# Kernel optimization log

Hardware: AMD Instinct MI355X
Metric: run time of the kernel (lower is better)

Reference implementation:

```python
import jax, jax.numpy as jnp
import numpy as np

N = 8192
D = 256  # hidden_size = in_features = out_features
NEG_SLOPE = 0.01  # nn.LeakyReLU() default
MASK_VAL = -1e12


def setup_inputs() -> dict:
    key = jax.random.key(0)
    k1, k2, k3, k4 = jax.random.split(key, 4)
    x = jax.random.normal(k1, (N, D), dtype=jnp.float32)
    adj = jax.random.randint(k2, (N, N), 0, 2, dtype=jnp.int32)
    # kaiming_uniform_ style params (scaled random uniform)
    W = jax.random.normal(k3, (D, D), dtype=jnp.float32) * (1.0 / np.sqrt(D))
    a = jax.random.normal(k4, (2 * D, 1), dtype=jnp.float32) * (1.0 / np.sqrt(2 * D))
    return {"x": x, "adj": adj, "W": W, "a": a}


def reference(x, adj, W, a):
    # GraphAttentionLayer.forward (eval mode: dropout is identity)
    h = x @ W  # [N, D]
    # a_input[i,j] = concat(h_i, h_j); a_input @ a decomposes as:
    #   e[i,j] = h_i . a[:D] + h_j . a[D:]
    # identical math without materializing the [N, N, 2D] tensor.
    e_src = h @ a[:D, 0]  # [N]
    e_dst = h @ a[D:, 0]  # [N]
    e = e_src[:, None] + e_dst[None, :]  # [N, N]
    e = jnp.where(e > 0, e, NEG_SLOPE * e)  # LeakyReLU
    att_logits = jnp.where(adj > 0, e, MASK_VAL)
    attention = jax.nn.softmax(att_logits, axis=1)
    h_prime = attention @ h  # [N, D]
    return jax.nn.elu(h_prime)  # concat=True branch
```

## Files before the change

### kernel.cpp

```cpp
#include <hip/hip_runtime.h>

#define NN 8192
#define DD 256
#define NSTEP (NN / 32)

typedef __attribute__((ext_vector_type(8))) short short8;
typedef __attribute__((ext_vector_type(4))) float f32x4;

__device__ __forceinline__ short f2bf(float x) {
    union { float f; unsigned u; } v; v.f = x;
    unsigned r = (v.u + 0x7FFFu + ((v.u >> 16) & 1u)) >> 16;
    return (short)r;
}
__device__ __forceinline__ float bf2f(short b) {
    union { float f; unsigned u; } v; v.u = ((unsigned)(unsigned short)b) << 16;
    return v.f;
}

__device__ __forceinline__ void barrier_keep_vmem() {
    asm volatile("s_waitcnt lgkmcnt(0)" ::: "memory");
    __builtin_amdgcn_s_barrier();
    asm volatile("" ::: "memory");
}

__global__ __launch_bounds__(256) void gat_pack(
    const int* __restrict__ adj, unsigned* __restrict__ bits)
{
    const int t   = threadIdx.x;
    const int row = blockIdx.x;
    const int* ar = adj + (size_t)row * NN;
    unsigned* br  = bits + (size_t)row * (NN / 32);
    #pragma unroll
    for (int i = 0; i < 8; ++i) {
        int j0 = i * 1024 + t * 4;
        int4 v = *(const int4*)(ar + j0);
        unsigned nib = (v.x > 0 ? 1u : 0u) | (v.y > 0 ? 2u : 0u)
                     | (v.z > 0 ? 4u : 0u) | (v.w > 0 ? 8u : 0u);
        unsigned word = nib << ((t & 7) * 4);
        word |= __shfl_xor((int)word, 1);
        word |= __shfl_xor((int)word, 2);
        word |= __shfl_xor((int)word, 4);
        if ((t & 7) == 0) br[i * 32 + (t >> 3)] = word;
    }
}

__global__ __launch_bounds__(256) void gat_prep(
    const float* __restrict__ x, const float* __restrict__ W,
    const float* __restrict__ a,
    short* __restrict__ hT, float* __restrict__ e_src, float* __restrict__ e_dst)
{
    __shared__ float x_s[32][260];
    __shared__ float W_s[2][16][256];
    const int t  = threadIdx.x;
    const int ib = blockIdx.x * 32;

    #pragma unroll
    for (int rep = 0; rep < 8; ++rep) {
        int fi = rep * 256 + t;
        int r  = fi >> 6;
        int c4 = (fi & 63) * 4;
        float4 v = *(const float4*)(x + (size_t)(ib + r) * DD + c4);
        *(float4*)&x_s[r][c4] = v;
    }
    float4 wp[4];
    #pragma unroll
    for (int q = 0; q < 4; ++q) {
        int fi = q * 256 + t;
        wp[q] = *(const float4*)(W + (size_t)(fi >> 6) * DD + (fi & 63) * 4);
    }
    barrier_keep_vmem();

    const int il = t >> 3;
    const int dg = (t & 7) * 4;
    f32x4 acc[8];
    #pragma unroll
    for (int m = 0; m < 8; ++m) acc[m] = (f32x4){0.f, 0.f, 0.f, 0.f};

    for (int kc = 0; kc < 16; ++kc) {
        const int b = kc & 1;
        #pragma unroll
        for (int q = 0; q < 4; ++q) {
            int fi = q * 256 + t;
            *(float4*)&W_s[b][fi >> 6][(fi & 63) * 4] = wp[q];
        }
        if (kc < 15) {
            #pragma unroll
            for (int q = 0; q < 4; ++q) {
                int fi = q * 256 + t;
                wp[q] = *(const float4*)(W + (size_t)((kc + 1) * 16 + (fi >> 6)) * DD + (fi & 63) * 4);
            }
        }
        barrier_keep_vmem();
        #pragma unroll
        for (int kl = 0; kl < 16; ++kl) {
            float xv = x_s[il][kc * 16 + kl];
            #pragma unroll
            for (int m = 0; m < 8; ++m) {
                float4 wv = *(const float4*)&W_s[b][kl][m * 32 + dg];
                acc[m].x += xv * wv.x; acc[m].y += xv * wv.y;
                acc[m].z += xv * wv.z; acc[m].w += xv * wv.w;
            }
        }
    }

    const int ig = ib + il;
    float p1 = 0.f, p2 = 0.f;
    #pragma unroll
    for (int m = 0; m < 8; ++m) {
        #pragma unroll
        for (int j = 0; j < 4; ++j) {
            int col = m * 32 + dg + j;
            float hv = acc[m][j];
            p1 += hv * a[col];
            p2 += hv * a[DD + col];
            hT[(size_t)col * NN + ig] = f2bf(hv);
        }
    }
    p1 += __shfl_xor(p1, 1); p1 += __shfl_xor(p1, 2); p1 += __shfl_xor(p1, 4);
    p2 += __shfl_xor(p2, 1); p2 += __shfl_xor(p2, 2); p2 += __shfl_xor(p2, 4);
    if ((t & 7) == 0) { e_src[ig] = p1; e_dst[ig] = p2; }
}

__global__ __launch_bounds__(512) void gat_main(
    const unsigned* __restrict__ bits, const short* __restrict__ hT,
    const float* __restrict__ e_src, const float* __restrict__ e_dst,
    float* __restrict__ out)
{
    __shared__ __align__(16) short w_s[2][32][40];
    __shared__ float denom_s[32];

    const int t    = threadIdx.x;
    const int lane = t & 63;
    const int wid  = t >> 6;
    const int ibl  = blockIdx.x * 32;

    const int irow = t >> 4;
    const int jc2  = (t & 15) * 2;
    const float es = e_src[ibl + irow];
    const unsigned* bits_row = bits + (size_t)(ibl + irow) * (NN / 32);

    const int cb   = wid * 32;
    const int arow = lane & 15;
    const int kg8  = (lane >> 4) * 8;
    const short* hB = hT + (size_t)(cb + arow) * NN + kg8;

    float dsum = 0.f;
    f32x4 acc00 = {0.f,0.f,0.f,0.f}, acc01 = acc00, acc10 = acc00, acc11 = acc00;

    unsigned bwA = bits_row[0];
    float2   edA = *(const float2*)(e_dst + jc2);
    int4     b0A = *(const int4*)(hB);
    int4     b1A = *(const int4*)(hB + 16 * NN);
    unsigned bwB = bits_row[1];
    float2   edB = *(const float2*)(e_dst + 32 + jc2);
    int4     b0B = *(const int4*)(hB + 32);
    int4     b1B = *(const int4*)(hB + 16 * NN + 32);

#define MAIN_STEP(BW, ED, B0, B1, n)                                           \
    {                                                                          \
        const int c = (n) & 1;                                                 \
        int4 g0 = B0, g1 = B1;                       \
        float s0 = es + ED.x, s1 = es + ED.y;                                  \
        float l0 = s0 > 0.f ? s0 : 0.01f * s0;                                 \
        float l1 = s1 > 0.f ? s1 : 0.01f * s1;                                 \
        float w0 = ((BW >> jc2) & 1u)       ? __expf(l0) : 0.f;                \
        float w1 = ((BW >> (jc2 + 1)) & 1u) ? __expf(l1) : 0.f;                \
        short b0 = f2bf(w0), b1 = f2bf(w1);                                    \
        dsum += bf2f(b0) + bf2f(b1);    \
        *(unsigned*)&w_s[c][irow][jc2] =                                       \
            (unsigned)(unsigned short)b0 | ((unsigned)(unsigned short)b1 << 16);\
        int jn = (((n) + 2) & (NSTEP - 1)) * 32;         \
        BW = bits_row[jn >> 5];                                                \
        ED = *(const float2*)(e_dst + jn + jc2);                               \
        B0 = *(const int4*)(hB + jn);                                          \
        B1 = *(const int4*)(hB + 16 * NN + jn);                                \
        barrier_keep_vmem();          \
        short8 a0 = *(const short8*)&w_s[c][arow][kg8];                        \
        short8 a1 = *(const short8*)&w_s[c][16 + arow][kg8];                   \
        acc00 = __builtin_amdgcn_mfma_f32_16x16x32_bf16(a0, *(short8*)&g0, acc00, 0, 0, 0);\
        acc01 = __builtin_amdgcn_mfma_f32_16x16x32_bf16(a0, *(short8*)&g1, acc01, 0, 0, 0);\
        acc10 = __builtin_amdgcn_mfma_f32_16x16x32_bf16(a1, *(short8*)&g0, acc10, 0, 0, 0);\
        acc11 = __builtin_amdgcn_mfma_f32_16x16x32_bf16(a1, *(short8*)&g1, acc11, 0, 0, 0);\
    }

    for (int n = 0; n < NSTEP; n += 2) {
        MAIN_STEP(bwA, edA, b0A, b1A, n)
        MAIN_STEP(bwB, edB, b0B, b1B, n + 1)
    }
#undef MAIN_STEP

    dsum += __shfl_xor(dsum, 1);
    dsum += __shfl_xor(dsum, 2);
    dsum += __shfl_xor(dsum, 4);
    dsum += __shfl_xor(dsum, 8);
    if ((t & 15) == 0) denom_s[irow] = dsum;
    __syncthreads();

    const int r4 = (lane >> 4) * 4;
    #pragma unroll
    for (int r = 0; r < 4; ++r) {
        float inv0 = 1.f / denom_s[r4 + r];
        float inv1 = 1.f / denom_s[16 + r4 + r];
        size_t o0 = (size_t)(ibl + r4 + r) * DD + cb + arow;
        size_t o1 = (size_t)(ibl + 16 + r4 + r) * DD + cb + arow;
        float v00 = acc00[r] * inv0; v00 = v00 > 0.f ? v00 : expm1f(v00);
        float v01 = acc01[r] * inv0; v01 = v01 > 0.f ? v01 : expm1f(v01);
        float v10 = acc10[r] * inv1; v10 = v10 > 0.f ? v10 : expm1f(v10);
        float v11 = acc11[r] * inv1; v11 = v11 > 0.f ? v11 : expm1f(v11);
        out[o0]      = v00;
        out[o0 + 16] = v01;
        out[o1]      = v10;
        out[o1 + 16] = v11;
    }
}

extern "C" void kernel_launch(void* const* d_in, const int* in_sizes, int n_in,
                              void* d_out, int out_size, void* d_ws, size_t ws_size,
                              hipStream_t stream) {
    const float* x   = (const float*)d_in[0];
    const int*   adj = (const int*)d_in[1];
    const float* W   = (const float*)d_in[2];
    const float* a   = (const float*)d_in[3];
    float* out = (float*)d_out;

    char* w0 = (char*)d_ws;
    short* hT      = (short*)w0;
    float* esrc    = (float*)(w0 + (size_t)DD * NN * 2);
    float* edst    = esrc + NN;
    unsigned* bits = (unsigned*)(edst + NN);

    gat_pack<<<dim3(NN), dim3(256), 0, stream>>>(adj, bits);
    gat_prep<<<dim3(NN / 32), dim3(256), 0, stream>>>(x, W, a, hT, esrc, edst);
    gat_main<<<dim3(NN / 32), dim3(512), 0, stream>>>(bits, hT, esrc, edst, out);
}
```

Baseline: 221.3 us.

## Split neighbor dimension across waves and reduce partial sums through LDS

Each wave now covers a disjoint eighth of the neighbor columns for all 256 output features, instead of a 32-column output slice across all neighbors. Every wave builds its attention-weight fragments directly in registers, so the per-step LDS write and block barrier go away. Partial accumulators and denominators are then summed across the eight waves through a large LDS exchange buffer before normalization and ELU. The cost is 32 accumulator tiles per lane, which strains registers under the new launch bound of two blocks per CU and may spill, plus a large LDS footprint that can limit occupancy.

Result: faster. 216.4 us (-2.2%).

```diff
diff --git a/kernel.cpp b/kernel.cpp
--- a/kernel.cpp
+++ b/kernel.cpp
@@ -2,7 +2,6 @@
 
 #define NN 8192
 #define DD 256
-#define NSTEP (NN / 32)
 
 typedef __attribute__((ext_vector_type(8))) short short8;
 typedef __attribute__((ext_vector_type(4))) float f32x4;
@@ -121,96 +120,123 @@
     if ((t & 7) == 0) { e_src[ig] = p1; e_dst[ig] = p2; }
 }
 
-__global__ __launch_bounds__(512) void gat_main(
+__global__ __launch_bounds__(512, 2) void gat_main(
     const unsigned* __restrict__ bits, const short* __restrict__ hT,
     const float* __restrict__ e_src, const float* __restrict__ e_dst,
     float* __restrict__ out)
 {
-    __shared__ __align__(16) short w_s[2][32][40];
-    __shared__ float denom_s[32];
+    __shared__ float xch[8][32][132];
+    __shared__ float denw[8][32];
 
     const int t    = threadIdx.x;
     const int lane = t & 63;
-    const int wid  = t >> 6;
+    const int w    = t >> 6;
     const int ibl  = blockIdx.x * 32;
 
-    const int irow = t >> 4;
-    const int jc2  = (t & 15) * 2;
-    const float es = e_src[ibl + irow];
-    const unsigned* bits_row = bits + (size_t)(ibl + irow) * (NN / 32);
-
-    const int cb   = wid * 32;
     const int arow = lane & 15;
     const int kg8  = (lane >> 4) * 8;
-    const short* hB = hT + (size_t)(cb + arow) * NN + kg8;
-
-    float dsum = 0.f;
-    f32x4 acc00 = {0.f,0.f,0.f,0.f}, acc01 = acc00, acc10 = acc00, acc11 = acc00;
-
-    unsigned bwA = bits_row[0];
-    float2   edA = *(const float2*)(e_dst + jc2);
-    int4     b0A = *(const int4*)(hB);
-    int4     b1A = *(const int4*)(hB + 16 * NN);
-    unsigned bwB = bits_row[1];
-    float2   edB = *(const float2*)(e_dst + 32 + jc2);
-    int4     b0B = *(const int4*)(hB + 32);
-    int4     b1B = *(const int4*)(hB + 16 * NN + 32);
-
-#define MAIN_STEP(BW, ED, B0, B1, n)                                           \
-    {                                                                          \
-        const int c = (n) & 1;                                                 \
-        int4 g0 = B0, g1 = B1;                       \
-        float s0 = es + ED.x, s1 = es + ED.y;                                  \
-        float l0 = s0 > 0.f ? s0 : 0.01f * s0;                                 \
-        float l1 = s1 > 0.f ? s1 : 0.01f * s1;                                 \
-        float w0 = ((BW >> jc2) & 1u)       ? __expf(l0) : 0.f;                \
-        float w1 = ((BW >> (jc2 + 1)) & 1u) ? __expf(l1) : 0.f;                \
-        short b0 = f2bf(w0), b1 = f2bf(w1);                                    \
-        dsum += bf2f(b0) + bf2f(b1);    \
-        *(unsigned*)&w_s[c][irow][jc2] =                                       \
-            (unsigned)(unsigned short)b0 | ((unsigned)(unsigned short)b1 << 16);\
-        int jn = (((n) + 2) & (NSTEP - 1)) * 32;         \
-        BW = bits_row[jn >> 5];                                                \
-        ED = *(const float2*)(e_dst + jn + jc2);                               \
-        B0 = *(const int4*)(hB + jn);                                          \
-        B1 = *(const int4*)(hB + 16 * NN + jn);                                \
-        barrier_keep_vmem();          \
-        short8 a0 = *(const short8*)&w_s[c][arow][kg8];                        \
-        short8 a1 = *(const short8*)&w_s[c][16 + arow][kg8];                   \
-        acc00 = __builtin_amdgcn_mfma_f32_16x16x32_bf16(a0, *(short8*)&g0, acc00, 0, 0, 0);\
-        acc01 = __builtin_amdgcn_mfma_f32_16x16x32_bf16(a0, *(short8*)&g1, acc01, 0, 0, 0);\
-        acc10 = __builtin_amdgcn_mfma_f32_16x16x32_bf16(a1, *(short8*)&g0, acc10, 0, 0, 0);\
-        acc11 = __builtin_amdgcn_mfma_f32_16x16x32_bf16(a1, *(short8*)&g1, acc11, 0, 0, 0);\
-    }
-
-    for (int n = 0; n < NSTEP; n += 2) {
-        MAIN_STEP(bwA, edA, b0A, b1A, n)
-        MAIN_STEP(bwB, edB, b0B, b1B, n + 1)
-    }
-#undef MAIN_STEP
-
-    dsum += __shfl_xor(dsum, 1);
-    dsum += __shfl_xor(dsum, 2);
-    dsum += __shfl_xor(dsum, 4);
-    dsum += __shfl_xor(dsum, 8);
-    if ((t & 15) == 0) denom_s[irow] = dsum;
+    const int jw   = w * (NN / 8);
+
+    const float es0 = e_src[ibl + arow];
+    const float es1 = e_src[ibl + 16 + arow];
+    const unsigned* br0 = bits + (size_t)(ibl + arow) * (NN / 32) + (jw >> 5);
+    const unsigned* br1 = br0 + 16 * (NN / 32);
+    const float* edp = e_dst + jw + kg8;
+    const short* hB  = hT + (size_t)arow * NN + jw + kg8;
+
+    f32x4 acc0[16], acc1[16];
+    #pragma unroll
+    for (int q = 0; q < 16; ++q) {
+        acc0[q] = (f32x4){0.f, 0.f, 0.f, 0.f};
+        acc1[q] = (f32x4){0.f, 0.f, 0.f, 0.f};
+    }
+    float dsum0 = 0.f, dsum1 = 0.f;
+
+    #pragma unroll 2
+    for (int n = 0; n < 32; ++n) {
+        const int j32 = n * 32;
+        unsigned bw0 = br0[n];
+        unsigned bw1 = br1[n];
+        float4 e0 = *(const float4*)(edp + j32);
+        float4 e1 = *(const float4*)(edp + j32 + 4);
+        int4 bq0[8], bq1[8];
+        #pragma unroll
+        for (int q = 0; q < 8; ++q)
+            bq0[q] = *(const int4*)(hB + (size_t)q * 16 * NN + j32);
+
+        short8 af0, af1;
+        float ed[8] = {e0.x, e0.y, e0.z, e0.w, e1.x, e1.y, e1.z, e1.w};
+        #pragma unroll
+        for (int i = 0; i < 8; ++i) {
+            float s0 = es0 + ed[i], s1 = es1 + ed[i];
+            float l0 = s0 > 0.f ? s0 : 0.01f * s0;
+            float l1 = s1 > 0.f ? s1 : 0.01f * s1;
+            float w0 = ((bw0 >> (kg8 + i)) & 1u) ? __expf(l0) : 0.f;
+            float w1 = ((bw1 >> (kg8 + i)) & 1u) ? __expf(l1) : 0.f;
+            short b0 = f2bf(w0), b1 = f2bf(w1);
+            af0[i] = b0; af1[i] = b1;
+            dsum0 += bf2f(b0);
+            dsum1 += bf2f(b1);
+        }
+
+        #pragma unroll
+        for (int q = 0; q < 8; ++q)
+            bq1[q] = *(const int4*)(hB + (size_t)(8 + q) * 16 * NN + j32);
+
+        #pragma unroll
+        for (int q = 0; q < 8; ++q) {
+            acc0[q] = __builtin_amdgcn_mfma_f32_16x16x32_bf16(af0, *(short8*)&bq0[q], acc0[q], 0, 0, 0);
+            acc1[q] = __builtin_amdgcn_mfma_f32_16x16x32_bf16(af1, *(short8*)&bq0[q], acc1[q], 0, 0, 0);
+        }
+        #pragma unroll
+        for (int q = 0; q < 8; ++q) {
+            acc0[8 + q] = __builtin_amdgcn_mfma_f32_16x16x32_bf16(af0, *(short8*)&bq1[q], acc0[8 + q], 0, 0, 0);
+            acc1[8 + q] = __builtin_amdgcn_mfma_f32_16x16x32_bf16(af1, *(short8*)&bq1[q], acc1[8 + q], 0, 0, 0);
+        }
+    }
+
+    dsum0 += __shfl_xor(dsum0, 16); dsum0 += __shfl_xor(dsum0, 32);
+    dsum1 += __shfl_xor(dsum1, 16); dsum1 += __shfl_xor(dsum1, 32);
+    if (lane < 16) { denw[w][lane] = dsum0; denw[w][16 + lane] = dsum1; }
     __syncthreads();
 
-    const int r4 = (lane >> 4) * 4;
-    #pragma unroll
-    for (int r = 0; r < 4; ++r) {
-        float inv0 = 1.f / denom_s[r4 + r];
-        float inv1 = 1.f / denom_s[16 + r4 + r];
-        size_t o0 = (size_t)(ibl + r4 + r) * DD + cb + arow;
-        size_t o1 = (size_t)(ibl + 16 + r4 + r) * DD + cb + arow;
-        float v00 = acc00[r] * inv0; v00 = v00 > 0.f ? v00 : expm1f(v00);
-        float v01 = acc01[r] * inv0; v01 = v01 > 0.f ? v01 : expm1f(v01);
-        float v10 = acc10[r] * inv1; v10 = v10 > 0.f ? v10 : expm1f(v10);
-        float v11 = acc11[r] * inv1; v11 = v11 > 0.f ? v11 : expm1f(v11);
-        out[o0]      = v00;
-        out[o0 + 16] = v01;
-        out[o1]      = v10;
-        out[o1 + 16] = v11;
+    const int ocol = lane & 15;
+    const int orow = (lane >> 4) * 4;
+    float inv[2][4];
+    #pragma unroll
+    for (int rh = 0; rh < 2; ++rh)
+        #pragma unroll
+        for (int i = 0; i < 4; ++i) {
+            int row = rh * 16 + orow + i;
+            float d = 0.f;
+            #pragma unroll
+            for (int sw = 0; sw < 8; ++sw) d += denw[sw][row];
+            inv[rh][i] = 1.f / d;
+        }
+
+    #pragma unroll
+    for (int p = 0; p < 2; ++p) {
+        __syncthreads();
+        #pragma unroll
+        for (int q = 0; q < 8; ++q)
+            #pragma unroll
+            for (int i = 0; i < 4; ++i) {
+                xch[w][orow + i][q * 16 + ocol]      = acc0[p * 8 + q][i];
+                xch[w][16 + orow + i][q * 16 + ocol] = acc1[p * 8 + q][i];
+            }
+        __syncthreads();
+        #pragma unroll
+        for (int rh = 0; rh < 2; ++rh)
+            #pragma unroll
+            for (int i = 0; i < 4; ++i) {
+                int row = rh * 16 + orow + i;
+                float s = 0.f;
+                #pragma unroll
+                for (int sw = 0; sw < 8; ++sw) s += xch[sw][row][w * 16 + ocol];
+                float v = s * inv[rh][i];
+                v = v > 0.f ? v : expm1f(v);
+                out[(size_t)(ibl + row) * DD + p * 128 + w * 16 + ocol] = v;
+            }
     }
 }
 
```
